# Optimization experiments

Hardware: AMD Instinct MI355X
Metric: run time of the kernel (lower is better)

## Reference

```python
import jax, jax.numpy as jnp
import numpy as np

B, DIM, KEY_DIM, NH, AR, RES, KS = 32, 512, 16, 8, 4, 64, 5
D = AR * KEY_DIM          # 64, per-head value dim
C4 = DIM // 4             # 128, q/k channel dim
CHUNK = DIM // NH         # 64, per-head input chunk
SCALE = KEY_DIM ** -0.5


def setup_inputs() -> dict:
    key = jax.random.key(0)
    ks = jax.random.split(key, 8)
    def rn(k, shape, fan):
        return jax.random.normal(k, shape, jnp.float32) * (fan ** -0.5)
    x = jax.random.normal(ks[0], (B, DIM, RES, RES), jnp.float32)
    qk_w = rn(ks[1], (DIM // 2, DIM), DIM)            # fused 1x1 conv+BN weight
    qk_b = jnp.zeros((DIM // 2,), jnp.float32)
    dws_w = rn(ks[2], (C4, 1, KS, KS), KS * KS)        # depthwise conv weight
    dws_b = jnp.zeros((C4,), jnp.float32)
    vs_w = rn(ks[3], (NH, D, CHUNK), CHUNK)            # per-head 1x1 conv weights
    vs_b = jnp.zeros((NH, D), jnp.float32)
    proj_w = rn(ks[4], (DIM, D * NH), D * NH)
    proj_b = jnp.zeros((DIM,), jnp.float32)
    bias_h = jax.random.normal(ks[5], (1, RES), jnp.float32) * 0.02
    bias_w = jax.random.normal(ks[6], (1, RES), jnp.float32) * 0.02
    # offset id for (p1, p2) is exactly |p1 - p2| given enumeration order
    idx = jnp.abs(jnp.arange(RES)[:, None] - jnp.arange(RES)[None, :]).astype(jnp.int32)
    return dict(x=x, qk_w=qk_w, qk_b=qk_b, dws_w=dws_w, dws_b=dws_b,
                vs_w=vs_w, vs_b=vs_b, proj_w=proj_w, proj_b=proj_b,
                bias_h=bias_h, bias_w=bias_w, idx_h=idx, idx_w=idx)


def reference(x, qk_w, qk_b, dws_w, dws_b, vs_w, vs_b, proj_w, proj_b,
              bias_h, bias_w, idx_h, idx_w):
    ab_h = bias_h[0][idx_h]                               # [N, N]
    ab_w = bias_w[0][idx_w]                               # [N, N]
    # qk: fused 1x1 conv + BN -> [B, C/2, H, W]
    feat = jnp.einsum('oc,bchw->bohw', qk_w, x) + qk_b[None, :, None, None]
    q, k = feat[:, :C4], feat[:, C4:]
    # depthwise 5x5 conv on q
    q = jax.lax.conv_general_dilated(
        q, dws_w, (1, 1), 'SAME',
        dimension_numbers=('NCHW', 'OIHW', 'NCHW'),
        feature_group_count=C4) + dws_b[None, :, None, None]
    qr_w = jnp.transpose(q, (0, 2, 3, 1))                 # [B, H, W, C4]
    kr_w = jnp.transpose(k, (0, 2, 3, 1))                 # [B, H, W, C4]
    attn_w = jax.nn.softmax(
        jnp.einsum('bhqc,bhkc->bhqk', qr_w, kr_w) * SCALE + ab_w, axis=-1)
    qr_h = jnp.transpose(qr_w, (0, 2, 1, 3))              # [B, W, H, C4]
    kr_h = jnp.transpose(kr_w, (0, 2, 1, 3))
    attn_h = jax.nn.softmax(
        jnp.einsum('bwqc,bwkc->bwqk', qr_h, kr_h) * SCALE + ab_h, axis=-1)
    # cascaded per-head value chain
    feats_out = []
    feat_i = x[:, :CHUNK]
    for i in range(NH):
        if i > 0:
            feat_i = feat_i + x[:, i * CHUNK:(i + 1) * CHUNK]
        v = jnp.einsum('dc,bchw->bdhw', vs_w[i], feat_i) + vs_b[i][None, :, None, None]
        v = jnp.transpose(v, (0, 2, 3, 1))                # [B, H, W, d]
        v = jnp.einsum('bhqk,bhkd->bhqd', attn_w, v)      # attend along W
        v = jnp.transpose(v, (0, 2, 1, 3))                # [B, W, H, d]
        f = jnp.einsum('bwqk,bwkd->bwqd', attn_h, v)      # attend along H
        feats_out.append(jnp.transpose(f, (0, 3, 2, 1)))  # [B, d, H, W]
    out = jnp.concatenate(feats_out, axis=1)              # [B, d*NH, H, W]
    out = jax.nn.relu(out)
    out = jnp.einsum('oc,bchw->bohw', proj_w, out) + proj_b[None, :, None, None]
    return out
```

## Files before the change

### kernel.cpp

```cpp
#include <hip/hip_runtime.h>

#define PIX 4096
#define SCALE 0.25f

typedef _Float16 f16x8 __attribute__((ext_vector_type(8)));
typedef float f32x4 __attribute__((ext_vector_type(4)));

__device__ inline void gload_lds16(const _Float16* g, _Float16* l) {
  __builtin_amdgcn_global_load_lds((const __attribute__((address_space(1))) void*)g,
                                   (__attribute__((address_space(3))) void*)l, 16, 0, 0);
}

__global__ __launch_bounds__(256) void k_cvt(const float* __restrict__ in,
                                             _Float16* __restrict__ out, int n) {
  int i = blockIdx.x * 256 + threadIdx.x;
  if (i < n) out[i] = (_Float16)in[i];
}

__global__ __launch_bounds__(256) void k_build_wbig(const float* __restrict__ vs_w,
                                                    _Float16* __restrict__ Wbig) {
  int row = blockIdx.x;
  int i = row >> 6, d = row & 63;
  for (int col = threadIdx.x; col < 512; col += 256) {
    int j = col >> 6, c = col & 63;
    Wbig[row * 512 + col] = (j <= i) ? (_Float16)vs_w[i * 4096 + d * 64 + c] : (_Float16)0;
  }
}

__global__ __launch_bounds__(256) void k_xt(const float* __restrict__ x,
                                            _Float16* __restrict__ xh) {
  __shared__ float tile[64][65];
  int b = blockIdx.z, k0 = blockIdx.y * 64, p0 = blockIdx.x * 64;
  const float* xp = x + ((size_t)b * 512 + k0) * PIX + p0;
  _Float16* out = xh + (size_t)b * PIX * 512;
  int t = threadIdx.x;
  int r = t >> 4, c4 = (t & 15) << 2;
#pragma unroll
  for (int it = 0; it < 4; ++it) {
    float4 v = *(const float4*)&xp[(size_t)(r + it * 16) * PIX + c4];
    tile[r + it * 16][c4 + 0] = v.x; tile[r + it * 16][c4 + 1] = v.y;
    tile[r + it * 16][c4 + 2] = v.z; tile[r + it * 16][c4 + 3] = v.w;
  }
  __syncthreads();
  int pr = t >> 5, kk = (t & 31) << 1;
#pragma unroll
  for (int it = 0; it < 8; ++it) {
    int p = pr + it * 8;
    union { _Float16 h[2]; unsigned int u; } pk;
    pk.h[0] = (_Float16)tile[kk][p]; pk.h[1] = (_Float16)tile[kk + 1][p];
    *(unsigned int*)&out[(size_t)(p0 + p) * 512 + k0 + kk] = pk.u;
  }
}

template<int MODE>
__global__ __launch_bounds__(256) void k_mgemm2(const _Float16* __restrict__ A,
                                                const _Float16* __restrict__ B,
                                                const float* __restrict__ bias,
                                                const _Float16* __restrict__ attn,
                                                float* C, _Float16* H, int nwg_m) {
  __shared__ __align__(16) char smem[34816];
  _Float16* As = (_Float16*)smem;
  _Float16* Bs = As + 8192;
  int nwg = gridDim.x;
  int id = blockIdx.x;
  int qq = nwg >> 3;
  id = (id & 7) * qq + (id >> 3);
  int mb = id % nwg_m;
  int rest = id / nwg_m;
  int pb = rest & 31;
  int b  = rest >> 5;
  int m0 = mb * 128, p0 = pb * 128;
  const _Float16* Bb = B + (size_t)b * 2097152;
  int t = threadIdx.x, wid = t >> 6, lane = t & 63;
  int wm = (wid >> 1) * 64, wn = (wid & 1) * 64;
  int lr = lane & 15, q = lane >> 4;
  f32x4 acc[4][4] = {};
  int kend = (MODE == 1) ? (m0 + 128) : 512;
  int nt = kend >> 5;
  int L0 = wid * 64 + lane, r0 = L0 >> 2, c0 = (L0 & 3) ^ ((r0 >> 1) & 3);
  int L1 = (4 + wid) * 64 + lane, r1 = L1 >> 2, c1 = (L1 & 3) ^ ((r1 >> 1) & 3);
  const _Float16* Ab = A + (size_t)m0 * 512;
  const _Float16* Bp = Bb + (size_t)p0 * 512;
  size_t ga0 = (size_t)r0 * 512 + c0 * 8, ga1 = (size_t)r1 * 512 + c1 * 8;
  gload_lds16(Ab + ga0, &As[wid * 512]);
  gload_lds16(Ab + ga1, &As[(4 + wid) * 512]);
  gload_lds16(Bp + ga0, &Bs[wid * 512]);
  gload_lds16(Bp + ga1, &Bs[(4 + wid) * 512]);
  __syncthreads();
  int cur = 0;
  for (int tt = 0; tt < nt; ++tt) {
    if (tt + 1 < nt) {
      int k0 = (tt + 1) << 5;
      gload_lds16(Ab + ga0 + k0, &As[(cur ^ 1) * 4096 + wid * 512]);
      gload_lds16(Ab + ga1 + k0, &As[(cur ^ 1) * 4096 + (4 + wid) * 512]);
      gload_lds16(Bp + ga0 + k0, &Bs[(cur ^ 1) * 4096 + wid * 512]);
      gload_lds16(Bp + ga1 + k0, &Bs[(cur ^ 1) * 4096 + (4 + wid) * 512]);
    }
    f16x8 af[4], bf_[4];
#pragma unroll
    for (int mi = 0; mi < 4; ++mi) {
      int rr = wm + mi * 16 + lr;
      af[mi] = *(const f16x8*)&As[cur * 4096 + rr * 32 + ((q ^ ((rr >> 1) & 3)) << 3)];
    }
#pragma unroll
    for (int ni = 0; ni < 4; ++ni) {
      int rr = wn + ni * 16 + lr;
      bf_[ni] = *(const f16x8*)&Bs[cur * 4096 + rr * 32 + ((q ^ ((rr >> 1) & 3)) << 3)];
    }
#pragma unroll
    for (int mi = 0; mi < 4; ++mi)
#pragma unroll
      for (int ni = 0; ni < 4; ++ni)
        acc[mi][ni] = __builtin_amdgcn_mfma_f32_16x16x32_f16(af[mi], bf_[ni], acc[mi][ni], 0, 0, 0);
    __syncthreads();
    cur ^= 1;
  }

  if (MODE == 0) {
#pragma unroll
    for (int mi = 0; mi < 4; ++mi)
#pragma unroll
      for (int rr = 0; rr < 4; ++rr) {
        int m = m0 + wm + mi * 16 + q * 4 + rr;
        float bi = bias[m];
        float* crow = C + ((size_t)b * 512 + m) * PIX + p0 + wn;
#pragma unroll
        for (int ni = 0; ni < 4; ++ni)
          crow[ni * 16 + lr] = acc[mi][ni][rr] + bi;
      }
  }

  if (MODE == 1) {
    _Float16* Cs = (_Float16*)smem + wid * 4096;
    int s = (p0 >> 6) + (wn >> 6);
    const _Float16* Ab2 = attn + ((size_t)b * 64 + s) * 4096;
    f16x8 bfr[4][2];
#pragma unroll
    for (int ni = 0; ni < 4; ++ni)
#pragma unroll
      for (int kk = 0; kk < 2; ++kk)
        bfr[ni][kk] = *(const f16x8*)&Ab2[(ni * 16 + lr) * 64 + q * 8 + kk * 32];
#pragma unroll
    for (int mi = 0; mi < 4; ++mi)
#pragma unroll
      for (int ni = 0; ni < 4; ++ni)
#pragma unroll
        for (int rr = 0; rr < 4; ++rr) {
          int row = mi * 16 + q * 4 + rr, col = ni * 16 + lr;
          Cs[row * 64 + ((((col >> 3) ^ (row & 7)) << 3) | (col & 7))] =
              (_Float16)(acc[mi][ni][rr] + bias[m0 + wm + row]);
        }
    f32x4 acc2[4][4] = {};
#pragma unroll
    for (int mi2 = 0; mi2 < 4; ++mi2)
#pragma unroll
      for (int kk = 0; kk < 2; ++kk) {
        f16x8 afr = *(const f16x8*)&Cs[(mi2 * 16 + lr) * 64 + (((q + kk * 4) ^ (lr & 7)) << 3)];
#pragma unroll
        for (int ni2 = 0; ni2 < 4; ++ni2)
          acc2[mi2][ni2] = __builtin_amdgcn_mfma_f32_16x16x32_f16(afr, bfr[ni2][kk], acc2[mi2][ni2], 0, 0, 0);
      }
#pragma unroll
    for (int mi2 = 0; mi2 < 4; ++mi2)
#pragma unroll
      for (int rr = 0; rr < 4; ++rr) {
        int m = m0 + wm + mi2 * 16 + q * 4 + rr;
        _Float16* crow = H + ((size_t)b * 512 + m) * PIX + p0 + wn;
#pragma unroll
        for (int ni2 = 0; ni2 < 4; ++ni2)
          crow[ni2 * 16 + lr] = (_Float16)acc2[mi2][ni2][rr];
      }
  }

  if (MODE == 2) {
    if (mb == 0) {
#pragma unroll
      for (int mi = 0; mi < 4; ++mi)
#pragma unroll
        for (int rr = 0; rr < 4; ++rr) {
          int m = wm + mi * 16 + q * 4 + rr;
          float bi = bias[m];
          float* crow = C + ((size_t)b * 128 + m) * PIX + p0 + wn;
#pragma unroll
          for (int ni = 0; ni < 4; ++ni)
            crow[ni * 16 + lr] = acc[mi][ni][rr] + bi;
        }
    } else {
      _Float16* Ts = (_Float16*)smem;
#pragma unroll
      for (int mi = 0; mi < 4; ++mi)
#pragma unroll
        for (int ni = 0; ni < 4; ++ni)
#pragma unroll
          for (int rr = 0; rr < 4; ++rr) {
            int row = mi * 16 + q * 4 + rr;
            Ts[(wn + ni * 16 + lr) * 136 + wm + row] =
                (_Float16)(acc[mi][ni][rr] + bias[m0 + wm + row]);
          }
      __syncthreads();
      _Float16* khb = H + ((size_t)b * PIX + p0) * 128;
#pragma unroll
      for (int it = 0; it < 8; ++it) {
        int idx = it * 256 + t;
        int row = idx >> 4, cc = (idx & 15) << 3;
        *(f16x8*)&khb[(size_t)row * 128 + cc] = *(const f16x8*)&Ts[row * 136 + cc];
      }
    }
  }
}

__global__ __launch_bounds__(256) void k_dwconv(const float* __restrict__ feat,
                                                const float* __restrict__ w,
                                                const float* __restrict__ bias,
                                                float* __restrict__ qconv) {
  __shared__ float tile[68][68];
  int c = blockIdx.x, b = blockIdx.y;
  const float* in = feat + ((size_t)b * 128 + c) * PIX;
  float wreg[25];
#pragma unroll
  for (int i = 0; i < 25; ++i) wreg[i] = w[c * 25 + i];
  float bi = bias[c];
  int t = threadIdx.x;
  for (int idx = t; idx < 68 * 68; idx += 256) {
    int y = idx / 68, xx = idx - y * 68;
    int h = y - 2, ww = xx - 2;
    float v = 0.f;
    if (h >= 0 && h < 64 && ww >= 0 && ww < 64) v = in[h * 64 + ww];
    tile[y][xx] = v;
  }
  __syncthreads();
  float* out = qconv + ((size_t)b * 128 + c) * PIX;
  int tx = (t & 15) << 2, ty = (t >> 4) << 2;
#pragma unroll
  for (int i = 0; i < 4; ++i) {
    float4 o;
    float* po = (float*)&o;
#pragma unroll
    for (int j = 0; j < 4; ++j) {
      float s = bi;
#pragma unroll
      for (int dy = 0; dy < 5; ++dy)
#pragma unroll
        for (int dx = 0; dx < 5; ++dx)
          s += wreg[dy * 5 + dx] * tile[ty + i + dy][tx + j + dx];
      po[j] = s;
    }
    *(float4*)&out[(ty + i) * 64 + tx] = o;
  }
}

__global__ __launch_bounds__(256) void k_qkt(const float* __restrict__ in, long ibs, int ic0,
                                             _Float16* __restrict__ out) {
  __shared__ __align__(16) _Float16 Ts[64 * 136];
  int p0 = blockIdx.x * 64, b = blockIdx.y;
  const float* ip = in + (size_t)b * ibs + (size_t)ic0 * PIX;
  int t = threadIdx.x;
#pragma unroll
  for (int it = 0; it < 8; ++it) {
    int i4 = it * 256 + t;
    int c = i4 >> 4, pp = (i4 & 15) << 2;
    float4 v = *(const float4*)&ip[(size_t)c * PIX + p0 + pp];
    Ts[(pp + 0) * 136 + c] = (_Float16)v.x;
    Ts[(pp + 1) * 136 + c] = (_Float16)v.y;
    Ts[(pp + 2) * 136 + c] = (_Float16)v.z;
    Ts[(pp + 3) * 136 + c] = (_Float16)v.w;
  }
  __syncthreads();
  _Float16* op = out + (size_t)b * (PIX * 128) + (size_t)p0 * 128;
#pragma unroll
  for (int it = 0; it < 4; ++it) {
    int ch = it * 256 + t;
    int p = ch >> 4, cc = (ch & 15) << 3;
    *(f16x8*)&op[p * 128 + cc] = *(const f16x8*)&Ts[p * 136 + cc];
  }
}

__global__ __launch_bounds__(256) void k_mattn(const _Float16* __restrict__ qh,
                                               const _Float16* __restrict__ kh,
                                               const float* __restrict__ bias_w,
                                               const float* __restrict__ bias_h,
                                               _Float16* __restrict__ attnW,
                                               _Float16* __restrict__ attnH) {
  __shared__ __align__(16) _Float16 Qs[64 * 136];
  __shared__ __align__(16) _Float16 Ks[64 * 136];
  __shared__ float bl[64];
  int j = blockIdx.x, b = blockIdx.y, which = blockIdx.z;
  const float* bias = which ? bias_h : bias_w;
  _Float16* attn = which ? attnH : attnW;
  int t = threadIdx.x;
  if (t < 64) bl[t] = bias[t];
  const _Float16* qb = qh + (size_t)b * (PIX * 128);
  const _Float16* kb = kh + (size_t)b * (PIX * 128);
#pragma unroll
  for (int it = 0; it < 4; ++it) {
    int idx = it * 256 + t;
    int r = idx >> 4, cc = (idx & 15) << 3;
    size_t p = which ? (size_t)(j + 64 * r) : (size_t)(j * 64 + r);
    *(f16x8*)&Qs[r * 136 + cc] = *(const f16x8*)&qb[p * 128 + cc];
    *(f16x8*)&Ks[r * 136 + cc] = *(const f16x8*)&kb[p * 128 + cc];
  }
  __syncthreads();
  int wave = t >> 6, lane = t & 63;
  int lr = lane & 15, q4 = lane >> 4;
  f16x8 af[4];
#pragma unroll
  for (int kk = 0; kk < 4; ++kk)
    af[kk] = *(const f16x8*)&Qs[(wave * 16 + lr) * 136 + q4 * 8 + kk * 32];
  f32x4 acc[4] = {};
#pragma unroll
  for (int ni = 0; ni < 4; ++ni)
#pragma unroll
    for (int kk = 0; kk < 4; ++kk) {
      f16x8 bf = *(const f16x8*)&Ks[(ni * 16 + lr) * 136 + q4 * 8 + kk * 32];
      acc[ni] = __builtin_amdgcn_mfma_f32_16x16x32_f16(af[kk], bf, acc[ni], 0, 0, 0);
    }
  float ev[4][4], sm[4];
#pragma unroll
  for (int r = 0; r < 4; ++r) {
    int qrow = wave * 16 + q4 * 4 + r;
    float m = -1e30f;
#pragma unroll
    for (int ni = 0; ni < 4; ++ni) {
      int k = ni * 16 + lr;
      ev[ni][r] = acc[ni][r] * SCALE + bl[abs(qrow - k)];
      m = fmaxf(m, ev[ni][r]);
    }
    m = fmaxf(m, __shfl_xor(m, 1)); m = fmaxf(m, __shfl_xor(m, 2));
    m = fmaxf(m, __shfl_xor(m, 4)); m = fmaxf(m, __shfl_xor(m, 8));
    float s = 0.f;
#pragma unroll
    for (int ni = 0; ni < 4; ++ni) { ev[ni][r] = __expf(ev[ni][r] - m); s += ev[ni][r]; }
    s += __shfl_xor(s, 1); s += __shfl_xor(s, 2);
    s += __shfl_xor(s, 4); s += __shfl_xor(s, 8);
    sm[r] = 1.f / s;
  }
  _Float16* ab = attn + (((size_t)b * 64 + j) * 64) * 64;
#pragma unroll
  for (int r = 0; r < 4; ++r) {
    int qrow = wave * 16 + q4 * 4 + r;
#pragma unroll
    for (int ni = 0; ni < 4; ++ni)
      ab[qrow * 64 + ni * 16 + lr] = (_Float16)(ev[ni][r] * sm[r]);
  }
}

__global__ __launch_bounds__(256) void k_hmix(const _Float16* __restrict__ tT,
                                              const _Float16* __restrict__ attnH,
                                              _Float16* __restrict__ ght) {
  __shared__ __align__(16) _Float16 Ts[128 * 64];
  __shared__ __align__(16) _Float16 Ls[64 * 136];
  int id = blockIdx.x;
  int ct = id & 3, w = (id >> 2) & 63, b = id >> 8;
  int t = threadIdx.x, wid = t >> 6, lane = t & 63;
  int lr = lane & 15, q4 = lane >> 4;
  const _Float16* Tb = tT + ((size_t)b * 512 + ct * 128) * PIX + w * 64;
#pragma unroll
  for (int it = 0; it < 4; ++it) {
    int idx = it * 256 + t;
    int row = idx >> 3, c = idx & 7;
    int sc = c ^ (row & 7);
    gload_lds16(Tb + (size_t)row * PIX + sc * 8, &Ts[(it * 256 + wid * 64) * 8]);
  }
  const _Float16* Ab = attnH + ((size_t)b * 64 + w) * 4096;
  f16x8 bfr[4][2];
#pragma unroll
  for (int ni = 0; ni < 4; ++ni)
#pragma unroll
    for (int kk = 0; kk < 2; ++kk)
      bfr[ni][kk] = *(const f16x8*)&Ab[(ni * 16 + lr) * 64 + q4 * 8 + kk * 32];
  __syncthreads();
  f32x4 acc[2][4] = {};
#pragma unroll
  for (int mi = 0; mi < 2; ++mi) {
    int rr = wid * 32 + mi * 16 + lr;
#pragma unroll
    for (int kk = 0; kk < 2; ++kk) {
      f16x8 af = *(const f16x8*)&Ts[rr * 64 + (((q4 + 4 * kk) ^ (rr & 7)) << 3)];
#pragma unroll
      for (int ni = 0; ni < 4; ++ni)
        acc[mi][ni] = __builtin_amdgcn_mfma_f32_16x16x32_f16(af, bfr[ni][kk], acc[mi][ni], 0, 0, 0);
    }
  }
#pragma unroll
  for (int mi = 0; mi < 2; ++mi)
#pragma unroll
    for (int ni = 0; ni < 4; ++ni)
#pragma unroll
      for (int rr = 0; rr < 4; ++rr) {
        float v = acc[mi][ni][rr];
        Ls[(ni * 16 + lr) * 136 + wid * 32 + mi * 16 + q4 * 4 + rr] =
            (_Float16)(v > 0.f ? v : 0.f);
      }
  __syncthreads();
  _Float16* gb = ght + (size_t)b * PIX * 512 + ct * 128;
#pragma unroll
  for (int it = 0; it < 4; ++it) {
    int idx = it * 256 + t;
    int hp = idx >> 4, cc = (idx & 15) << 3;
    *(f16x8*)&gb[((size_t)hp * 64 + w) * 512 + cc] = *(const f16x8*)&Ls[hp * 136 + cc];
  }
}

__global__ __launch_bounds__(256) void k_t16(const _Float16* __restrict__ in,
                                             _Float16* __restrict__ out) {
  __shared__ _Float16 tile[64][65];
  int img = blockIdx.x;
  const _Float16* ip = in + (size_t)img * PIX;
  _Float16* op = out + (size_t)img * PIX;
  int t = threadIdx.x;
  int col = t & 63, r0 = t >> 6;
  for (int it = 0; it < 16; ++it) {
    int r = r0 + it * 4;
    tile[r][col] = ip[r * 64 + col];
  }
  __syncthreads();
  for (int it = 0; it < 16; ++it) {
    int r = r0 + it * 4;
    op[r * 64 + col] = tile[col][r];
  }
}

extern "C" void kernel_launch(void* const* d_in, const int* in_sizes, int n_in,
                              void* d_out, int out_size, void* d_ws, size_t ws_size,
                              hipStream_t stream) {
  const float* x      = (const float*)d_in[0];
  const float* qk_w   = (const float*)d_in[1];
  const float* qk_b   = (const float*)d_in[2];
  const float* dws_w  = (const float*)d_in[3];
  const float* dws_b  = (const float*)d_in[4];
  const float* vs_w   = (const float*)d_in[5];
  const float* vs_b   = (const float*)d_in[6];
  const float* proj_w = (const float*)d_in[7];
  const float* proj_b = (const float*)d_in[8];
  const float* bias_h = (const float*)d_in[9];
  const float* bias_w = (const float*)d_in[10];

  float* ws = (float*)d_ws;
  float* dout = (float*)d_out;

  _Float16* xh    = (_Float16*)ws;
  _Float16* ght   = xh;
  float*    feat  = ws + 33554432;
  _Float16* tT    = (_Float16*)(ws + 33554432);
  _Float16* attnW = (_Float16*)(ws + 67108864);
  _Float16* attnH = (_Float16*)(ws + 71303168);
  _Float16* qkw_h  = (_Float16*)(ws + 75497472);
  _Float16* wbig_h = (_Float16*)(ws + 75563008);
  _Float16* pjw_h  = (_Float16*)(ws + 75694080);

  float*    qconv = dout;
  _Float16* qh    = (_Float16*)(dout + 16777216);
  _Float16* kh    = (_Float16*)(dout + 25165824);
  _Float16* Vh    = (_Float16*)(dout + 33554432);

  k_cvt<<<dim3(512), 256, 0, stream>>>(qk_w, qkw_h, 131072);
  k_cvt<<<dim3(1024), 256, 0, stream>>>(proj_w, pjw_h, 262144);
  k_build_wbig<<<512, 256, 0, stream>>>(vs_w, wbig_h);
  k_xt<<<dim3(64, 8, 32), 256, 0, stream>>>(x, xh);
  k_mgemm2<2><<<2048, 256, 0, stream>>>(qkw_h, xh, qk_b, nullptr, feat, kh, 2);
  k_dwconv<<<dim3(128, 32), 256, 0, stream>>>(feat, dws_w, dws_b, qconv);
  k_qkt<<<dim3(64, 32), 256, 0, stream>>>(qconv, 128L * PIX, 0, qh);
  k_mattn<<<dim3(64, 32, 2), 256, 0, stream>>>(qh, kh, bias_w, bias_h, attnW, attnH);
  k_mgemm2<1><<<4096, 256, 0, stream>>>(wbig_h, xh, vs_b, attnW, nullptr, Vh, 4);
  k_t16<<<32 * 512, 256, 0, stream>>>(Vh, tT);
  k_hmix<<<8192, 256, 0, stream>>>(tT, attnH, ght);
  k_mgemm2<0><<<4096, 256, 0, stream>>>(pjw_h, ght, proj_b, nullptr, dout, nullptr, 4);
}
```

Before: 659.9 us.

## Enlarge GEMM tiles to 256x256 with 8 waves and 4-stage LDS pipeline

```diff
diff --git a/kernel.cpp b/kernel.cpp
--- a/kernel.cpp
+++ b/kernel.cpp
@@ -53,77 +53,86 @@
 }
 
 template<int MODE>
-__global__ __launch_bounds__(256) void k_mgemm2(const _Float16* __restrict__ A,
+__global__ __launch_bounds__(512, 2) void k_mg8(const _Float16* __restrict__ A,
                                                 const _Float16* __restrict__ B,
                                                 const float* __restrict__ bias,
                                                 const _Float16* __restrict__ attn,
                                                 float* C, _Float16* H, int nwg_m) {
-  __shared__ __align__(16) char smem[34816];
-  _Float16* As = (_Float16*)smem;
-  _Float16* Bs = As + 8192;
+  __shared__ __align__(16) _Float16 lds[65536];
   int nwg = gridDim.x;
   int id = blockIdx.x;
   int qq = nwg >> 3;
   id = (id & 7) * qq + (id >> 3);
   int mb = id % nwg_m;
   int rest = id / nwg_m;
-  int pb = rest & 31;
-  int b  = rest >> 5;
-  int m0 = mb * 128, p0 = pb * 128;
-  const _Float16* Bb = B + (size_t)b * 2097152;
+  int pb = rest & 15;
+  int b  = rest >> 4;
+  int m0 = mb * 256, p0 = pb * 256;
   int t = threadIdx.x, wid = t >> 6, lane = t & 63;
-  int wm = (wid >> 1) * 64, wn = (wid & 1) * 64;
-  int lr = lane & 15, q = lane >> 4;
-  f32x4 acc[4][4] = {};
-  int kend = (MODE == 1) ? (m0 + 128) : 512;
-  int nt = kend >> 5;
-  int L0 = wid * 64 + lane, r0 = L0 >> 2, c0 = (L0 & 3) ^ ((r0 >> 1) & 3);
-  int L1 = (4 + wid) * 64 + lane, r1 = L1 >> 2, c1 = (L1 & 3) ^ ((r1 >> 1) & 3);
+  int wm = wid >> 2, wn = wid & 3;
+  int lr = lane & 15, q4 = lane >> 4;
   const _Float16* Ab = A + (size_t)m0 * 512;
-  const _Float16* Bp = Bb + (size_t)p0 * 512;
-  size_t ga0 = (size_t)r0 * 512 + c0 * 8, ga1 = (size_t)r1 * 512 + c1 * 8;
-  gload_lds16(Ab + ga0, &As[wid * 512]);
-  gload_lds16(Ab + ga1, &As[(4 + wid) * 512]);
-  gload_lds16(Bp + ga0, &Bs[wid * 512]);
-  gload_lds16(Bp + ga1, &Bs[(4 + wid) * 512]);
-  __syncthreads();
-  int cur = 0;
-  for (int tt = 0; tt < nt; ++tt) {
-    if (tt + 1 < nt) {
-      int k0 = (tt + 1) << 5;
-      gload_lds16(Ab + ga0 + k0, &As[(cur ^ 1) * 4096 + wid * 512]);
-      gload_lds16(Ab + ga1 + k0, &As[(cur ^ 1) * 4096 + (4 + wid) * 512]);
-      gload_lds16(Bp + ga0 + k0, &Bs[(cur ^ 1) * 4096 + wid * 512]);
-      gload_lds16(Bp + ga1 + k0, &Bs[(cur ^ 1) * 4096 + (4 + wid) * 512]);
-    }
-    f16x8 af[4], bf_[4];
-#pragma unroll
-    for (int mi = 0; mi < 4; ++mi) {
-      int rr = wm + mi * 16 + lr;
-      af[mi] = *(const f16x8*)&As[cur * 4096 + rr * 32 + ((q ^ ((rr >> 1) & 3)) << 3)];
+  const _Float16* Bp = B + (size_t)b * 2097152 + (size_t)p0 * 512;
+
+  int nt = (MODE == 1) ? ((m0 + 256) >> 6) : 8;
+  int nsub = nt * 2;
+
+  auto STAGE = [&](int g) {
+    int slot = g & 3;
+    _Float16* dA = lds + slot * 16384;
+    _Float16* dB = dA + 8192;
+    size_t ks = (size_t)g * 32;
+#pragma unroll
+    for (int is = 0; is < 2; ++is) {
+      int L = is * 512 + wid * 64 + lane;
+      int row = L >> 2, sl = L & 3;
+      int c = sl ^ ((row >> 1) & 3);
+      gload_lds16(Ab + (size_t)row * 512 + ks + c * 8, dA + (size_t)(is * 512 + wid * 64) * 8);
+      gload_lds16(Bp + (size_t)row * 512 + ks + c * 8, dB + (size_t)(is * 512 + wid * 64) * 8);
+    }
+  };
+
+  f32x4 acc[8][4] = {};
+  STAGE(0); STAGE(1); STAGE(2);
+  for (int n = 0; n < nsub; ++n) {
+    if (n + 3 < nsub) STAGE(n + 3);
+    int r = nsub - 1 - n; if (r > 3) r = 3;
+    if (r == 3)      asm volatile("s_waitcnt vmcnt(12)" ::: "memory");
+    else if (r == 2) asm volatile("s_waitcnt vmcnt(8)" ::: "memory");
+    else if (r == 1) asm volatile("s_waitcnt vmcnt(4)" ::: "memory");
+    else             asm volatile("s_waitcnt vmcnt(0)" ::: "memory");
+    __builtin_amdgcn_s_barrier();
+    const _Float16* A_s = lds + (n & 3) * 16384;
+    const _Float16* B_s = A_s + 8192;
+    f16x8 af[8], bf[4];
+#pragma unroll
+    for (int mi = 0; mi < 8; ++mi) {
+      int row = wm * 128 + mi * 16 + lr;
+      af[mi] = *(const f16x8*)&A_s[row * 32 + ((q4 ^ ((row >> 1) & 3)) << 3)];
     }
 #pragma unroll
     for (int ni = 0; ni < 4; ++ni) {
-      int rr = wn + ni * 16 + lr;
-      bf_[ni] = *(const f16x8*)&Bs[cur * 4096 + rr * 32 + ((q ^ ((rr >> 1) & 3)) << 3)];
-    }
-#pragma unroll
-    for (int mi = 0; mi < 4; ++mi)
+      int row = wn * 64 + ni * 16 + lr;
+      bf[ni] = *(const f16x8*)&B_s[row * 32 + ((q4 ^ ((row >> 1) & 3)) << 3)];
+    }
+    __builtin_amdgcn_s_setprio(1);
+#pragma unroll
+    for (int mi = 0; mi < 8; ++mi)
 #pragma unroll
       for (int ni = 0; ni < 4; ++ni)
-        acc[mi][ni] = __builtin_amdgcn_mfma_f32_16x16x32_f16(af[mi], bf_[ni], acc[mi][ni], 0, 0, 0);
-    __syncthreads();
-    cur ^= 1;
+        acc[mi][ni] = __builtin_amdgcn_mfma_f32_16x16x32_f16(af[mi], bf[ni], acc[mi][ni], 0, 0, 0);
+    __builtin_amdgcn_s_setprio(0);
+    __builtin_amdgcn_s_barrier();
   }
 
   if (MODE == 0) {
 #pragma unroll
-    for (int mi = 0; mi < 4; ++mi)
+    for (int mi = 0; mi < 8; ++mi)
 #pragma unroll
       for (int rr = 0; rr < 4; ++rr) {
-        int m = m0 + wm + mi * 16 + q * 4 + rr;
+        int m = m0 + wm * 128 + mi * 16 + q4 * 4 + rr;
         float bi = bias[m];
-        float* crow = C + ((size_t)b * 512 + m) * PIX + p0 + wn;
+        float* crow = C + ((size_t)b * 512 + m) * PIX + p0 + wn * 64;
 #pragma unroll
         for (int ni = 0; ni < 4; ++ni)
           crow[ni * 16 + lr] = acc[mi][ni][rr] + bi;
@@ -131,41 +140,43 @@
   }
 
   if (MODE == 1) {
-    _Float16* Cs = (_Float16*)smem + wid * 4096;
-    int s = (p0 >> 6) + (wn >> 6);
+    _Float16* Cs = lds + wid * 8192;
+#pragma unroll
+    for (int mi = 0; mi < 8; ++mi)
+#pragma unroll
+      for (int ni = 0; ni < 4; ++ni)
+#pragma unroll
+        for (int rr = 0; rr < 4; ++rr) {
+          int row = mi * 16 + q4 * 4 + rr;
+          int col = ni * 16 + lr;
+          Cs[row * 64 + ((((col >> 3) ^ (row & 7)) << 3) | (col & 7))] =
+              (_Float16)(acc[mi][ni][rr] + bias[m0 + wm * 128 + row]);
+        }
+    int s = pb * 4 + wn;
     const _Float16* Ab2 = attn + ((size_t)b * 64 + s) * 4096;
     f16x8 bfr[4][2];
 #pragma unroll
     for (int ni = 0; ni < 4; ++ni)
 #pragma unroll
       for (int kk = 0; kk < 2; ++kk)
-        bfr[ni][kk] = *(const f16x8*)&Ab2[(ni * 16 + lr) * 64 + q * 8 + kk * 32];
-#pragma unroll
-    for (int mi = 0; mi < 4; ++mi)
-#pragma unroll
-      for (int ni = 0; ni < 4; ++ni)
-#pragma unroll
-        for (int rr = 0; rr < 4; ++rr) {
-          int row = mi * 16 + q * 4 + rr, col = ni * 16 + lr;
-          Cs[row * 64 + ((((col >> 3) ^ (row & 7)) << 3) | (col & 7))] =
-              (_Float16)(acc[mi][ni][rr] + bias[m0 + wm + row]);
-        }
-    f32x4 acc2[4][4] = {};
-#pragma unroll
-    for (int mi2 = 0; mi2 < 4; ++mi2)
+        bfr[ni][kk] = *(const f16x8*)&Ab2[(ni * 16 + lr) * 64 + q4 * 8 + kk * 32];
+    f32x4 acc2[8][4] = {};
+#pragma unroll
+    for (int mi2 = 0; mi2 < 8; ++mi2)
 #pragma unroll
       for (int kk = 0; kk < 2; ++kk) {
-        f16x8 afr = *(const f16x8*)&Cs[(mi2 * 16 + lr) * 64 + (((q + kk * 4) ^ (lr & 7)) << 3)];
+        int row = mi2 * 16 + lr;
+        f16x8 afr = *(const f16x8*)&Cs[row * 64 + (((q4 + kk * 4) ^ (row & 7)) << 3)];
 #pragma unroll
         for (int ni2 = 0; ni2 < 4; ++ni2)
           acc2[mi2][ni2] = __builtin_amdgcn_mfma_f32_16x16x32_f16(afr, bfr[ni2][kk], acc2[mi2][ni2], 0, 0, 0);
       }
 #pragma unroll
-    for (int mi2 = 0; mi2 < 4; ++mi2)
+    for (int mi2 = 0; mi2 < 8; ++mi2)
 #pragma unroll
       for (int rr = 0; rr < 4; ++rr) {
-        int m = m0 + wm + mi2 * 16 + q * 4 + rr;
-        _Float16* crow = H + ((size_t)b * 512 + m) * PIX + p0 + wn;
+        int m = m0 + wm * 128 + mi2 * 16 + q4 * 4 + rr;
+        _Float16* crow = H + ((size_t)b * 512 + m) * PIX + p0 + wn * 64;
 #pragma unroll
         for (int ni2 = 0; ni2 < 4; ++ni2)
           crow[ni2 * 16 + lr] = (_Float16)acc2[mi2][ni2][rr];
@@ -173,37 +184,35 @@
   }
 
   if (MODE == 2) {
-    if (mb == 0) {
-#pragma unroll
-      for (int mi = 0; mi < 4; ++mi)
+    if (wm == 0) {
+#pragma unroll
+      for (int mi = 0; mi < 8; ++mi)
 #pragma unroll
         for (int rr = 0; rr < 4; ++rr) {
-          int m = wm + mi * 16 + q * 4 + rr;
+          int m = mi * 16 + q4 * 4 + rr;
           float bi = bias[m];
-          float* crow = C + ((size_t)b * 128 + m) * PIX + p0 + wn;
+          float* crow = C + ((size_t)b * 128 + m) * PIX + p0 + wn * 64;
 #pragma unroll
           for (int ni = 0; ni < 4; ++ni)
             crow[ni * 16 + lr] = acc[mi][ni][rr] + bi;
         }
     } else {
-      _Float16* Ts = (_Float16*)smem;
-#pragma unroll
-      for (int mi = 0; mi < 4; ++mi)
+      _Float16* Ls = lds + (size_t)(wid - 4) * 16384;
+#pragma unroll
+      for (int mi = 0; mi < 8; ++mi)
 #pragma unroll
         for (int ni = 0; ni < 4; ++ni)
 #pragma unroll
           for (int rr = 0; rr < 4; ++rr) {
-            int row = mi * 16 + q * 4 + rr;
-            Ts[(wn + ni * 16 + lr) * 136 + wm + row] =
-                (_Float16)(acc[mi][ni][rr] + bias[m0 + wm + row]);
+            int ch = mi * 16 + q4 * 4 + rr;
+            Ls[(ni * 16 + lr) * 136 + ch] = (_Float16)(acc[mi][ni][rr] + bias[128 + ch]);
           }
-      __syncthreads();
-      _Float16* khb = H + ((size_t)b * PIX + p0) * 128;
-#pragma unroll
-      for (int it = 0; it < 8; ++it) {
-        int idx = it * 256 + t;
-        int row = idx >> 4, cc = (idx & 15) << 3;
-        *(f16x8*)&khb[(size_t)row * 128 + cc] = *(const f16x8*)&Ts[row * 136 + cc];
+      _Float16* khb = H + ((size_t)b * PIX + p0 + wn * 64) * 128;
+#pragma unroll
+      for (int it = 0; it < 16; ++it) {
+        int chk = it * 64 + lane;
+        int prow = chk >> 4, cc = (chk & 15) << 3;
+        *(f16x8*)&khb[(size_t)prow * 128 + cc] = *(const f16x8*)&Ls[prow * 136 + cc];
       }
     }
   }
@@ -457,12 +466,12 @@
   k_cvt<<<dim3(1024), 256, 0, stream>>>(proj_w, pjw_h, 262144);
   k_build_wbig<<<512, 256, 0, stream>>>(vs_w, wbig_h);
   k_xt<<<dim3(64, 8, 32), 256, 0, stream>>>(x, xh);
-  k_mgemm2<2><<<2048, 256, 0, stream>>>(qkw_h, xh, qk_b, nullptr, feat, kh, 2);
+  k_mg8<2><<<512, 512, 0, stream>>>(qkw_h, xh, qk_b, nullptr, feat, kh, 1);
   k_dwconv<<<dim3(128, 32), 256, 0, stream>>>(feat, dws_w, dws_b, qconv);
   k_qkt<<<dim3(64, 32), 256, 0, stream>>>(qconv, 128L * PIX, 0, qh);
   k_mattn<<<dim3(64, 32, 2), 256, 0, stream>>>(qh, kh, bias_w, bias_h, attnW, attnH);
-  k_mgemm2<1><<<4096, 256, 0, stream>>>(wbig_h, xh, vs_b, attnW, nullptr, Vh, 4);
+  k_mg8<1><<<1024, 512, 0, stream>>>(wbig_h, xh, vs_b, attnW, nullptr, Vh, 2);
   k_t16<<<32 * 512, 256, 0, stream>>>(Vh, tT);
   k_hmix<<<8192, 256, 0, stream>>>(tT, attnH, ght);
-  k_mgemm2<0><<<4096, 256, 0, stream>>>(pjw_h, ght, proj_b, nullptr, dout, nullptr, 4);
-}
+  k_mg8<0><<<1024, 512, 0, stream>>>(pjw_h, ght, proj_b, nullptr, dout, nullptr, 2);
+}
```

New measurement: 601.5 us. -8.9%, faster.
